# Kernel optimization log

Measured on AMD Instinct MI355X. Metric: run time of the kernel, lower is better.

The kernel has to match this reference:

```python
import jax, jax.numpy as jnp
import numpy as np

B, C, H, W = 4, 512, 64, 64
D = 512  # model_dim


def setup_inputs() -> dict:
    key = jax.random.key(0)
    ks = jax.random.split(key, 9)
    s = 0.02
    return {
        "q": jax.random.normal(ks[0], (B, C, H, W), dtype=jnp.float32),
        "Wq": jax.random.normal(ks[1], (D, C), dtype=jnp.float32) * s,
        "bq": jax.random.normal(ks[2], (D,), dtype=jnp.float32) * s,
        "Wk": jax.random.normal(ks[3], (D, C), dtype=jnp.float32) * s,
        "bk": jax.random.normal(ks[4], (D,), dtype=jnp.float32) * s,
        "Wv": jax.random.normal(ks[5], (D, C), dtype=jnp.float32) * s,
        "bv": jax.random.normal(ks[6], (D,), dtype=jnp.float32) * s,
        "Wo": jax.random.normal(ks[7], (C, D), dtype=jnp.float32) * s,
        "bo": jax.random.normal(ks[8], (C,), dtype=jnp.float32) * s,
    }


def reference(q, Wq, bq, Wk, bk, Wv, bv, Wo, bo):
    b, c, h, w = q.shape
    # 1x1 conv == per-pixel linear over channels; tokens s = h*w
    x = q.reshape(b, c, h * w)                      # (b, c, s)
    Q = jnp.einsum('bcs,dc->bsd', x, Wq) + bq       # (b, s, D)
    K = jnp.einsum('bcs,dc->bsd', x, Wk) + bk
    V = jnp.einsum('bcs,dc->bsd', x, Wv) + bv
    # ScaleAttend: scale = q.shape[-1]^-0.5 = model_dim^-0.5 (heads not split)
    scale = jnp.asarray(Q.shape[-1], Q.dtype) ** -0.5
    sim = jnp.einsum('bsd,btd->bst', Q, K) * scale  # (b, s, s)
    attn = jax.nn.softmax(sim, axis=-1)
    o = jnp.einsum('bst,btd->bsd', attn, V)         # (b, s, D)
    # to_out 1x1 conv: D -> C
    y = jnp.einsum('bsd,cd->bsc', o, Wo) + bo       # (b, s, C)
    return y.transpose(0, 2, 1).reshape(b, c, h, w)
```

## Files before the change

kernel.cpp:

```cpp
#include <hip/hip_runtime.h>
#include <hip/hip_bf16.h>

typedef __hip_bfloat16 bf16;
typedef __attribute__((ext_vector_type(8))) short short8;
typedef __attribute__((ext_vector_type(4))) float floatx4;
typedef __attribute__((ext_vector_type(4))) short shortx4;

static constexpr int BATCH = 4;
static constexpr int CH    = 512;
static constexpr int SEQ   = 4096;
static constexpr int DM    = 512;

__device__ __forceinline__ void gload16(const void* g, void* l) {
  __builtin_amdgcn_global_load_lds(
      (const __attribute__((address_space(1))) unsigned int*)g,
      (__attribute__((address_space(3))) unsigned int*)l,
      16, 0, 0);
}

__global__ __launch_bounds__(256) void cvt_weights(
    const float* __restrict__ w0, const float* __restrict__ w1,
    const float* __restrict__ w2, const float* __restrict__ w3,
    bf16* __restrict__ out) {
  const float* src = (blockIdx.y == 0) ? w0 : (blockIdx.y == 1) ? w1
                   : (blockIdx.y == 2) ? w2 : w3;
  int idx = blockIdx.x * 256 + threadIdx.x;
  out[(long)blockIdx.y * (DM * CH) + idx] = __float2bfloat16(src[idx]);
}

__global__ __launch_bounds__(256) void transpose_cvt(
    const float* __restrict__ x, bf16* __restrict__ xT) {
  __shared__ float tile[64][65];
  const int s0 = blockIdx.x * 64, c0 = blockIdx.y * 64;
  const float* xb = x + (long)blockIdx.z * CH * SEQ;
  bf16* xTb = xT + (long)blockIdx.z * SEQ * CH;
  const int t = threadIdx.x;
  const int sl = t & 63, cq = t >> 6;
  #pragma unroll
  for (int i = 0; i < 16; ++i) {
    int cl = cq * 16 + i;
    tile[cl][sl] = xb[(long)(c0 + cl) * SEQ + s0 + sl];
  }
  __syncthreads();
  const int cl2 = t & 63, sq = t >> 6;
  #pragma unroll
  for (int i = 0; i < 16; ++i) {
    int sl2 = sq * 16 + i;
    xTb[(long)(s0 + sl2) * CH + c0 + cl2] = __float2bfloat16(tile[cl2][sl2]);
  }
}

template <int MODE>
__global__ __launch_bounds__(256) void gemm_bt(
    const bf16* __restrict__ A, long sAz,
    const bf16* __restrict__ B, long sBz,
    void* __restrict__ Cv, long sCz,
    const float* __restrict__ bias, float scale,
    int M, int N, int K, int ldc) {
  __shared__ bf16 At[128 * 32];
  __shared__ bf16 Bt[128 * 32];
  const int tid = threadIdx.x;
  const int z = blockIdx.z;
  const long lK = K;
  const bf16* Ab = A + (long)z * sAz + (long)blockIdx.y * 128 * lK;
  const bf16* Bb = B + (long)z * sBz + (long)blockIdx.x * 128 * lK;

  const int w = tid >> 6, lane = tid & 63;
  const int wm = (w & 1) << 6, wn = (w >> 1) << 6;
  const int l16 = lane & 15, quad = lane >> 4;

  floatx4 acc[4][4];
  #pragma unroll
  for (int i = 0; i < 4; ++i)
    #pragma unroll
    for (int j = 0; j < 4; ++j) acc[i][j] = (floatx4)(0.0f);

  const int row0 = tid >> 2;
  const int col0 = (tid & 3) << 3;
  const int nk = K >> 5;
  for (int kt = 0; kt < nk; ++kt) {
    const bf16* Ak = Ab + (kt << 5);
    const bf16* Bk = Bb + (kt << 5);
    gload16(Ak + (long)row0 * lK + col0,        (char*)At + tid * 16);
    gload16(Ak + (long)(row0 + 64) * lK + col0, (char*)At + (tid + 256) * 16);
    gload16(Bk + (long)row0 * lK + col0,        (char*)Bt + tid * 16);
    gload16(Bk + (long)(row0 + 64) * lK + col0, (char*)Bt + (tid + 256) * 16);
    __syncthreads();
    short8 af[4], bfr[4];
    #pragma unroll
    for (int i = 0; i < 4; ++i)
      af[i] = *(const short8*)(At + (wm + i * 16 + l16) * 32 + (quad << 3));
    #pragma unroll
    for (int j = 0; j < 4; ++j)
      bfr[j] = *(const short8*)(Bt + (wn + j * 16 + l16) * 32 + (quad << 3));
    #pragma unroll
    for (int i = 0; i < 4; ++i)
      #pragma unroll
      for (int j = 0; j < 4; ++j)
        acc[i][j] = __builtin_amdgcn_mfma_f32_16x16x32_bf16(af[i], bfr[j],
                                                            acc[i][j], 0, 0, 0);
    __syncthreads();
  }

  const int mbase = blockIdx.y * 128 + wm + quad * 4;
  const int nbase = blockIdx.x * 128 + wn + l16;
  #pragma unroll
  for (int i = 0; i < 4; ++i) {
    const int row = mbase + i * 16;
    #pragma unroll
    for (int j = 0; j < 4; ++j) {
      const int col = nbase + j * 16;
      floatx4 v = acc[i][j];
      if constexpr (MODE == 0) {
        bf16* C = (bf16*)Cv + (long)z * sCz;
        const float bb = bias[col];
        #pragma unroll
        for (int r = 0; r < 4; ++r)
          C[(long)(row + r) * ldc + col] = __float2bfloat16(v[r] + bb);
      } else if constexpr (MODE == 1) {
        bf16* C = (bf16*)Cv + (long)z * sCz;
        const float bb = bias[col];
        alignas(8) bf16 tmp[4];
        #pragma unroll
        for (int r = 0; r < 4; ++r) tmp[r] = __float2bfloat16(v[r] + bb);
        *(shortx4*)(C + (long)col * ldc + row) = *(const shortx4*)tmp;
      } else {
        float* C = (float*)Cv + (long)z * sCz;
        const float bb = bias[col];
        floatx4 o_;
        #pragma unroll
        for (int r = 0; r < 4; ++r) o_[r] = v[r] + bb;
        *(floatx4*)(C + (long)col * ldc + row) = o_;
      }
    }
  }
}

template <int NREP>
__global__ __launch_bounds__(512, 2) void gemm_big(
    const bf16* __restrict__ A, long sAz,
    const bf16* __restrict__ B, long sBz,
    bf16* __restrict__ C, long sCz,
    float scale, int K, int ldc) {
  constexpr int BN = NREP * 64;
  constexpr int NJ = NREP / 2;
  constexpr int BROUNDS = BN / 64;
  __shared__ __align__(16) bf16 As[2][256 * 64];
  __shared__ __align__(16) bf16 Bs[2][BN * 64];

  int id = blockIdx.x + gridDim.x * (blockIdx.y + gridDim.y * blockIdx.z);
  int nwg = gridDim.x * gridDim.y * gridDim.z;
  int sid = ((nwg & 7) == 0) ? ((id & 7) * (nwg >> 3) + (id >> 3)) : id;
  const int bx = sid % gridDim.x;
  const int by = (sid / gridDim.x) % gridDim.y;
  const int bz = sid / (gridDim.x * gridDim.y);

  const int tid = threadIdx.x;
  const long lK = K;
  const bf16* Ab = A + (long)bz * sAz + (long)by * 256 * lK;
  const bf16* Bb = B + (long)bz * sBz + (long)bx * BN * lK;

  const int w = tid >> 6, lane = tid & 63;
  const int wr = w >> 2, wc = w & 3;
  const int l16 = lane & 15, quad = lane >> 4;

  const int srow = tid >> 3;
  const int sp = tid & 7;
  const int slog = (sp ^ (srow & 7)) << 3;

  const int pA0 = (quad ^ (l16 & 7)) << 3;
  const int pA1 = pA0 ^ 32;

  auto stageA = [&](int buf, int kt) {
    const bf16* s = Ab + (long)kt * 64 + (long)srow * lK + slog;
    char* d = (char*)(&As[buf][0]) + tid * 16;
    #pragma unroll
    for (int r = 0; r < 4; ++r)
      gload16(s + (long)(r * 64) * lK, d + r * 8192);
  };
  auto stageB = [&](int buf, int kt) {
    const bf16* s = Bb + (long)kt * 64 + (long)srow * lK + slog;
    char* d = (char*)(&Bs[buf][0]) + tid * 16;
    #pragma unroll
    for (int r = 0; r < BROUNDS; ++r)
      gload16(s + (long)(r * 64) * lK, d + r * 8192);
  };

  floatx4 acc[8][NREP];
  #pragma unroll
  for (int m = 0; m < 8; ++m)
    #pragma unroll
    for (int n = 0; n < NREP; ++n) acc[m][n] = (floatx4)(0.0f);

  stageA(0, 0);
  stageB(0, 0);
  asm volatile("s_waitcnt vmcnt(0)" ::: "memory");
  __builtin_amdgcn_s_barrier();

  const int nk = K >> 6;
  int cur = 0;
  for (int t = 0; t < nk; ++t) {
    const bf16* __restrict__ Al = &As[cur][0];
    const bf16* __restrict__ Bl = &Bs[cur][0];
    const bool last = (t == nk - 1);
    short8 a0[4], a1[4], b0[NJ], b1[NJ];
    #pragma unroll
    for (int qm = 0; qm < 2; ++qm) {
      #pragma unroll
      for (int i = 0; i < 4; ++i) {
        const int ar = wr * 128 + qm * 64 + i * 16 + l16;
        const bf16* pa = Al + ar * 64;
        a0[i] = *(const short8*)(pa + pA0);
        a1[i] = *(const short8*)(pa + pA1);
      }
      #pragma unroll
      for (int qn = 0; qn < 2; ++qn) {
        #pragma unroll
        for (int j = 0; j < NJ; ++j) {
          const int br = wc * (NREP * 16) + qn * (NJ * 16) + j * 16 + l16;
          const bf16* pb = Bl + br * 64;
          b0[j] = *(const short8*)(pb + pA0);
          b1[j] = *(const short8*)(pb + pA1);
        }
        if (!last) {
          if (qm == 0 && qn == 0) stageA(cur ^ 1, t + 1);
          if (qm == 0 && qn == 1) stageB(cur ^ 1, t + 1);
        }
        __builtin_amdgcn_s_barrier();
        __builtin_amdgcn_s_setprio(1);
        #pragma unroll
        for (int i = 0; i < 4; ++i)
          #pragma unroll
          for (int j = 0; j < NJ; ++j) {
            const int m = qm * 4 + i, n = qn * NJ + j;
            acc[m][n] = __builtin_amdgcn_mfma_f32_16x16x32_bf16(
                a0[i], b0[j], acc[m][n], 0, 0, 0);
            acc[m][n] = __builtin_amdgcn_mfma_f32_16x16x32_bf16(
                a1[i], b1[j], acc[m][n], 0, 0, 0);
          }
        __builtin_amdgcn_s_setprio(0);
        if (qm == 1 && qn == 1) {
          asm volatile("s_waitcnt vmcnt(0)" ::: "memory");
        }
        __builtin_amdgcn_s_barrier();
      }
    }
    cur ^= 1;
  }

  bf16* Cb = C + (long)bz * sCz;
  const int rbase = by * 256 + wr * 128 + quad * 4;
  const int cbase = bx * BN + wc * (NREP * 16) + l16;
  #pragma unroll
  for (int m = 0; m < 8; ++m) {
    const int row = rbase + m * 16;
    #pragma unroll
    for (int n = 0; n < NREP; ++n) {
      const int col = cbase + n * 16;
      floatx4 v = acc[m][n];
      #pragma unroll
      for (int r = 0; r < 4; ++r)
        Cb[(long)(row + r) * ldc + col] = __float2bfloat16(v[r] * scale);
    }
  }
}

__global__ __launch_bounds__(256) void softmax_rows(bf16* __restrict__ sim) {
  bf16* p = sim + (long)blockIdx.y * ((long)SEQ * SEQ) + (long)blockIdx.x * SEQ;
  uint4* p4 = (uint4*)p;
  const int t = threadIdx.x;
  union U { uint4 u; ushort h[8]; } d[2];
  d[0].u = p4[t];
  d[1].u = p4[t + 256];
  float v[16];
  float mx = -3.0e38f;
  #pragma unroll
  for (int i = 0; i < 16; ++i) {
    v[i] = __uint_as_float(((unsigned)d[i >> 3].h[i & 7]) << 16);
    mx = fmaxf(mx, v[i]);
  }
  #pragma unroll
  for (int o = 32; o > 0; o >>= 1) mx = fmaxf(mx, __shfl_xor(mx, o));
  __shared__ float redmax[4], redsum[4];
  if ((t & 63) == 0) redmax[t >> 6] = mx;
  __syncthreads();
  mx = fmaxf(fmaxf(redmax[0], redmax[1]), fmaxf(redmax[2], redmax[3]));
  float sum = 0.f;
  #pragma unroll
  for (int i = 0; i < 16; ++i) {
    v[i] = __expf(v[i] - mx);
    sum += v[i];
  }
  #pragma unroll
  for (int o = 32; o > 0; o >>= 1) sum += __shfl_xor(sum, o);
  if ((t & 63) == 0) redsum[t >> 6] = sum;
  __syncthreads();
  sum = redsum[0] + redsum[1] + redsum[2] + redsum[3];
  const float inv = 1.0f / sum;
  union Hb { __hip_bfloat16 h; ushort u; };
  #pragma unroll
  for (int i = 0; i < 16; ++i) {
    Hb hb;
    hb.h = __float2bfloat16(v[i] * inv);
    d[i >> 3].h[i & 7] = hb.u;
  }
  p4[t] = d[0].u;
  p4[t + 256] = d[1].u;
}

extern "C" void kernel_launch(void* const* d_in, const int* in_sizes, int n_in,
                              void* d_out, int out_size, void* d_ws,
                              size_t ws_size, hipStream_t stream) {
  const float* q  = (const float*)d_in[0];
  const float* Wq = (const float*)d_in[1];
  const float* bq = (const float*)d_in[2];
  const float* Wk = (const float*)d_in[3];
  const float* bk = (const float*)d_in[4];
  const float* Wv = (const float*)d_in[5];
  const float* bv = (const float*)d_in[6];
  const float* Wo = (const float*)d_in[7];
  const float* bo = (const float*)d_in[8];
  float* out = (float*)d_out;

  bf16* ws = (bf16*)d_ws;
  const long WSZ = (long)DM * CH;
  const long XSZ = (long)SEQ * CH;
  const long SSZ = (long)SEQ * SEQ;
  bf16* Wqb = ws;
  bf16* Wkb = Wqb + WSZ;
  bf16* Wvb = Wqb + 2 * WSZ;
  bf16* Wob = Wqb + 3 * WSZ;
  bf16* xT  = Wqb + 4 * WSZ;
  bf16* Qb  = xT + BATCH * XSZ;
  bf16* Kb  = Qb + BATCH * XSZ;
  bf16* Vt  = Kb + BATCH * XSZ;
  bf16* Ob  = Vt + BATCH * XSZ;
  bf16* Sim = Ob + BATCH * XSZ;

  cvt_weights<<<dim3(WSZ / 256, 4), 256, 0, stream>>>(Wq, Wk, Wv, Wo, ws);
  transpose_cvt<<<dim3(SEQ / 64, CH / 64, BATCH), 256, 0, stream>>>(q, xT);

  gemm_bt<0><<<dim3(4, 32, BATCH), 256, 0, stream>>>(
      xT, XSZ, Wqb, 0, Qb, XSZ, bq, 1.f, SEQ, DM, CH, DM);
  gemm_bt<0><<<dim3(4, 32, BATCH), 256, 0, stream>>>(
      xT, XSZ, Wkb, 0, Kb, XSZ, bk, 1.f, SEQ, DM, CH, DM);
  gemm_bt<1><<<dim3(4, 32, BATCH), 256, 0, stream>>>(
      xT, XSZ, Wvb, 0, Vt, XSZ, bv, 1.f, SEQ, DM, CH, SEQ);
  gemm_big<4><<<dim3(16, 16, BATCH), 512, 0, stream>>>(
      Qb, XSZ, Kb, XSZ, Sim, SSZ, 0.04419417382415922f, CH, SEQ);
  softmax_rows<<<dim3(SEQ, BATCH), 256, 0, stream>>>(Sim);
  gemm_big<2><<<dim3(4, 16, BATCH), 512, 0, stream>>>(
      Sim, SSZ, Vt, XSZ, Ob, XSZ, 1.0f, SEQ, DM);
  gemm_bt<4><<<dim3(4, 32, BATCH), 256, 0, stream>>>(
      Ob, XSZ, Wob, 0, out, XSZ, bo, 1.f, SEQ, CH, DM, SEQ);
}
```

Before: 396.6 us.

## Route projection GEMMs through the big pipelined kernel and restructure its inner loop

Removes the simple 128x128 single-buffered gemm_bt kernel and runs the Q/K/V and output projections through gemm_big, which uses a 256-row tile, double-buffered LDS staging and a bias/transpose epilogue selected by a MODE template parameter. The inner k-loop of gemm_big is also reorganised into four phases, each covering one k-half and one M-half. All B fragments for a k-half are loaded once and reused across both M-halves, rather than being reloaded for every M and N quarter. The projections now launch fewer, larger workgroups (256 per GEMM), which may underfill the GPU. Holding b[2][NREP] fragments also raises register pressure.

```diff
diff --git a/kernel.cpp b/kernel.cpp
--- a/kernel.cpp
+++ b/kernel.cpp
@@ -50,100 +50,14 @@
   }
 }
 
-template <int MODE>
-__global__ __launch_bounds__(256) void gemm_bt(
+template <int NREP, int MODE>
+__global__ __launch_bounds__(512, 2) void gemm_big(
     const bf16* __restrict__ A, long sAz,
     const bf16* __restrict__ B, long sBz,
     void* __restrict__ Cv, long sCz,
     const float* __restrict__ bias, float scale,
-    int M, int N, int K, int ldc) {
-  __shared__ bf16 At[128 * 32];
-  __shared__ bf16 Bt[128 * 32];
-  const int tid = threadIdx.x;
-  const int z = blockIdx.z;
-  const long lK = K;
-  const bf16* Ab = A + (long)z * sAz + (long)blockIdx.y * 128 * lK;
-  const bf16* Bb = B + (long)z * sBz + (long)blockIdx.x * 128 * lK;
-
-  const int w = tid >> 6, lane = tid & 63;
-  const int wm = (w & 1) << 6, wn = (w >> 1) << 6;
-  const int l16 = lane & 15, quad = lane >> 4;
-
-  floatx4 acc[4][4];
-  #pragma unroll
-  for (int i = 0; i < 4; ++i)
-    #pragma unroll
-    for (int j = 0; j < 4; ++j) acc[i][j] = (floatx4)(0.0f);
-
-  const int row0 = tid >> 2;
-  const int col0 = (tid & 3) << 3;
-  const int nk = K >> 5;
-  for (int kt = 0; kt < nk; ++kt) {
-    const bf16* Ak = Ab + (kt << 5);
-    const bf16* Bk = Bb + (kt << 5);
-    gload16(Ak + (long)row0 * lK + col0,        (char*)At + tid * 16);
-    gload16(Ak + (long)(row0 + 64) * lK + col0, (char*)At + (tid + 256) * 16);
-    gload16(Bk + (long)row0 * lK + col0,        (char*)Bt + tid * 16);
-    gload16(Bk + (long)(row0 + 64) * lK + col0, (char*)Bt + (tid + 256) * 16);
-    __syncthreads();
-    short8 af[4], bfr[4];
-    #pragma unroll
-    for (int i = 0; i < 4; ++i)
-      af[i] = *(const short8*)(At + (wm + i * 16 + l16) * 32 + (quad << 3));
-    #pragma unroll
-    for (int j = 0; j < 4; ++j)
-      bfr[j] = *(const short8*)(Bt + (wn + j * 16 + l16) * 32 + (quad << 3));
-    #pragma unroll
-    for (int i = 0; i < 4; ++i)
-      #pragma unroll
-      for (int j = 0; j < 4; ++j)
-        acc[i][j] = __builtin_amdgcn_mfma_f32_16x16x32_bf16(af[i], bfr[j],
-                                                            acc[i][j], 0, 0, 0);
-    __syncthreads();
-  }
-
-  const int mbase = blockIdx.y * 128 + wm + quad * 4;
-  const int nbase = blockIdx.x * 128 + wn + l16;
-  #pragma unroll
-  for (int i = 0; i < 4; ++i) {
-    const int row = mbase + i * 16;
-    #pragma unroll
-    for (int j = 0; j < 4; ++j) {
-      const int col = nbase + j * 16;
-      floatx4 v = acc[i][j];
-      if constexpr (MODE == 0) {
-        bf16* C = (bf16*)Cv + (long)z * sCz;
-        const float bb = bias[col];
-        #pragma unroll
-        for (int r = 0; r < 4; ++r)
-          C[(long)(row + r) * ldc + col] = __float2bfloat16(v[r] + bb);
-      } else if constexpr (MODE == 1) {
-        bf16* C = (bf16*)Cv + (long)z * sCz;
-        const float bb = bias[col];
-        alignas(8) bf16 tmp[4];
-        #pragma unroll
-        for (int r = 0; r < 4; ++r) tmp[r] = __float2bfloat16(v[r] + bb);
-        *(shortx4*)(C + (long)col * ldc + row) = *(const shortx4*)tmp;
-      } else {
-        float* C = (float*)Cv + (long)z * sCz;
-        const float bb = bias[col];
-        floatx4 o_;
-        #pragma unroll
-        for (int r = 0; r < 4; ++r) o_[r] = v[r] + bb;
-        *(floatx4*)(C + (long)col * ldc + row) = o_;
-      }
-    }
-  }
-}
-
-template <int NREP>
-__global__ __launch_bounds__(512, 2) void gemm_big(
-    const bf16* __restrict__ A, long sAz,
-    const bf16* __restrict__ B, long sBz,
-    bf16* __restrict__ C, long sCz,
-    float scale, int K, int ldc) {
+    int K, int ldc) {
   constexpr int BN = NREP * 64;
-  constexpr int NJ = NREP / 2;
   constexpr int BROUNDS = BN / 64;
   __shared__ __align__(16) bf16 As[2][256 * 64];
   __shared__ __align__(16) bf16 Bs[2][BN * 64];
@@ -203,52 +117,45 @@
     const bf16* __restrict__ Al = &As[cur][0];
     const bf16* __restrict__ Bl = &Bs[cur][0];
     const bool last = (t == nk - 1);
-    short8 a0[4], a1[4], b0[NJ], b1[NJ];
-    #pragma unroll
-    for (int qm = 0; qm < 2; ++qm) {
+    short8 a[4];
+    short8 b[2][NREP];
+    #pragma unroll
+    for (int p = 0; p < 4; ++p) {
+      const int qm = p >> 1, kc = p & 1;
+      const int poff = kc ? pA1 : pA0;
       #pragma unroll
       for (int i = 0; i < 4; ++i) {
         const int ar = wr * 128 + qm * 64 + i * 16 + l16;
-        const bf16* pa = Al + ar * 64;
-        a0[i] = *(const short8*)(pa + pA0);
-        a1[i] = *(const short8*)(pa + pA1);
-      }
+        a[i] = *(const short8*)(Al + ar * 64 + poff);
+      }
+      if (qm == 0) {
+        #pragma unroll
+        for (int j = 0; j < NREP; ++j) {
+          const int br = wc * (NREP * 16) + j * 16 + l16;
+          b[kc][j] = *(const short8*)(Bl + br * 64 + poff);
+        }
+      }
+      if (!last) {
+        if (p == 0) stageA(cur ^ 1, t + 1);
+        if (p == 1) stageB(cur ^ 1, t + 1);
+      }
+      __builtin_amdgcn_s_barrier();
+      __builtin_amdgcn_s_setprio(1);
       #pragma unroll
-      for (int qn = 0; qn < 2; ++qn) {
-        #pragma unroll
-        for (int j = 0; j < NJ; ++j) {
-          const int br = wc * (NREP * 16) + qn * (NJ * 16) + j * 16 + l16;
-          const bf16* pb = Bl + br * 64;
-          b0[j] = *(const short8*)(pb + pA0);
-          b1[j] = *(const short8*)(pb + pA1);
-        }
-        if (!last) {
-          if (qm == 0 && qn == 0) stageA(cur ^ 1, t + 1);
-          if (qm == 0 && qn == 1) stageB(cur ^ 1, t + 1);
-        }
-        __builtin_amdgcn_s_barrier();
-        __builtin_amdgcn_s_setprio(1);
-        #pragma unroll
-        for (int i = 0; i < 4; ++i)
-          #pragma unroll
-          for (int j = 0; j < NJ; ++j) {
-            const int m = qm * 4 + i, n = qn * NJ + j;
-            acc[m][n] = __builtin_amdgcn_mfma_f32_16x16x32_bf16(
-                a0[i], b0[j], acc[m][n], 0, 0, 0);
-            acc[m][n] = __builtin_amdgcn_mfma_f32_16x16x32_bf16(
-                a1[i], b1[j], acc[m][n], 0, 0, 0);
-          }
-        __builtin_amdgcn_s_setprio(0);
-        if (qm == 1 && qn == 1) {
-          asm volatile("s_waitcnt vmcnt(0)" ::: "memory");
-        }
-        __builtin_amdgcn_s_barrier();
-      }
+      for (int i = 0; i < 4; ++i)
+        #pragma unroll
+        for (int j = 0; j < NREP; ++j)
+          acc[qm * 4 + i][j] = __builtin_amdgcn_mfma_f32_16x16x32_bf16(
+              a[i], b[kc][j], acc[qm * 4 + i][j], 0, 0, 0);
+      __builtin_amdgcn_s_setprio(0);
+      if (p == 3) {
+        asm volatile("s_waitcnt vmcnt(0)" ::: "memory");
+      }
+      __builtin_amdgcn_s_barrier();
     }
     cur ^= 1;
   }
 
-  bf16* Cb = C + (long)bz * sCz;
   const int rbase = by * 256 + wr * 128 + quad * 4;
   const int cbase = bx * BN + wc * (NREP * 16) + l16;
   #pragma unroll
@@ -258,9 +165,32 @@
     for (int n = 0; n < NREP; ++n) {
       const int col = cbase + n * 16;
       floatx4 v = acc[m][n];
-      #pragma unroll
-      for (int r = 0; r < 4; ++r)
-        Cb[(long)(row + r) * ldc + col] = __float2bfloat16(v[r] * scale);
+      if constexpr (MODE == 0) {
+        bf16* C = (bf16*)Cv + (long)bz * sCz;
+        const float bb = bias[col];
+        #pragma unroll
+        for (int r = 0; r < 4; ++r)
+          C[(long)(row + r) * ldc + col] = __float2bfloat16(v[r] + bb);
+      } else if constexpr (MODE == 1) {
+        bf16* C = (bf16*)Cv + (long)bz * sCz;
+        const float bb = bias[col];
+        alignas(8) bf16 tmp[4];
+        #pragma unroll
+        for (int r = 0; r < 4; ++r) tmp[r] = __float2bfloat16(v[r] + bb);
+        *(shortx4*)(C + (long)col * ldc + row) = *(const shortx4*)tmp;
+      } else if constexpr (MODE == 2) {
+        bf16* C = (bf16*)Cv + (long)bz * sCz;
+        #pragma unroll
+        for (int r = 0; r < 4; ++r)
+          C[(long)(row + r) * ldc + col] = __float2bfloat16(v[r] * scale);
+      } else {
+        float* C = (float*)Cv + (long)bz * sCz;
+        const float bb = bias[col];
+        floatx4 o_;
+        #pragma unroll
+        for (int r = 0; r < 4; ++r) o_[r] = v[r] + bb;
+        *(floatx4*)(C + (long)col * ldc + row) = o_;
+      }
     }
   }
 }
@@ -340,17 +270,17 @@
   cvt_weights<<<dim3(WSZ / 256, 4), 256, 0, stream>>>(Wq, Wk, Wv, Wo, ws);
   transpose_cvt<<<dim3(SEQ / 64, CH / 64, BATCH), 256, 0, stream>>>(q, xT);
 
-  gemm_bt<0><<<dim3(4, 32, BATCH), 256, 0, stream>>>(
-      xT, XSZ, Wqb, 0, Qb, XSZ, bq, 1.f, SEQ, DM, CH, DM);
-  gemm_bt<0><<<dim3(4, 32, BATCH), 256, 0, stream>>>(
-      xT, XSZ, Wkb, 0, Kb, XSZ, bk, 1.f, SEQ, DM, CH, DM);
-  gemm_bt<1><<<dim3(4, 32, BATCH), 256, 0, stream>>>(
-      xT, XSZ, Wvb, 0, Vt, XSZ, bv, 1.f, SEQ, DM, CH, SEQ);
-  gemm_big<4><<<dim3(16, 16, BATCH), 512, 0, stream>>>(
-      Qb, XSZ, Kb, XSZ, Sim, SSZ, 0.04419417382415922f, CH, SEQ);
+  gemm_big<2, 0><<<dim3(4, 16, BATCH), 512, 0, stream>>>(
+      xT, XSZ, Wqb, 0, Qb, XSZ, bq, 1.f, CH, DM);
+  gemm_big<2, 0><<<dim3(4, 16, BATCH), 512, 0, stream>>>(
+      xT, XSZ, Wkb, 0, Kb, XSZ, bk, 1.f, CH, DM);
+  gemm_big<2, 1><<<dim3(4, 16, BATCH), 512, 0, stream>>>(
+      xT, XSZ, Wvb, 0, Vt, XSZ, bv, 1.f, CH, SEQ);
+  gemm_big<4, 2><<<dim3(16, 16, BATCH), 512, 0, stream>>>(
+      Qb, XSZ, Kb, XSZ, Sim, SSZ, nullptr, 0.04419417382415922f, CH, SEQ);
   softmax_rows<<<dim3(SEQ, BATCH), 256, 0, stream>>>(Sim);
-  gemm_big<2><<<dim3(4, 16, BATCH), 512, 0, stream>>>(
-      Sim, SSZ, Vt, XSZ, Ob, XSZ, 1.0f, SEQ, DM);
-  gemm_bt<4><<<dim3(4, 32, BATCH), 256, 0, stream>>>(
-      Ob, XSZ, Wob, 0, out, XSZ, bo, 1.f, SEQ, CH, DM, SEQ);
-}
+  gemm_big<2, 2><<<dim3(4, 16, BATCH), 512, 0, stream>>>(
+      Sim, SSZ, Vt, XSZ, Ob, XSZ, nullptr, 1.0f, SEQ, DM);
+  gemm_big<2, 4><<<dim3(4, 16, BATCH), 512, 0, stream>>>(
+      Ob, XSZ, Wob, 0, out, XSZ, bo, 1.f, DM, SEQ);
+}
```

Result: faster. 382.1 us (-3.7%).
